# Kernel optimization log

Hardware: AMD Instinct MI355X
Metric: run time of the kernel (lower is better)

The kernel has to match this reference:

```python
import jax, jax.numpy as jnp
import numpy as np
from jax import lax

H = 12  # num_heads

def conv1d_same(x, w, b):
    # x: [B, Cin, L], w: [Cout, Cin, K] (torch Conv1d layout), 'same' padding
    y = lax.conv_general_dilated(x, w, window_strides=(1,), padding='SAME',
                                 dimension_numbers=('NCH', 'OIH', 'NCH'))
    return y + b[None, :, None]

def setup_inputs() -> dict:
    key = jax.random.key(0)
    ks = jax.random.split(key, 16)
    B, N, C = 8, 4096, 768
    d = C // H
    s = 0.02
    return {
        'x': jax.random.normal(ks[0], (B, N, C), dtype=jnp.float32),
        'qkv_w': jax.random.normal(ks[1], (3 * C, C), dtype=jnp.float32) * s,
        'proj_w': jax.random.normal(ks[2], (C, C), dtype=jnp.float32) * s,
        'proj_b': jnp.zeros((C,), dtype=jnp.float32),
        'conv_w': jax.random.normal(ks[3], (d, d, 5), dtype=jnp.float32) * s,  # k=5 from log2(768)
        'conv_b': jnp.zeros((d,), dtype=jnp.float32),
        'fc_w': jax.random.normal(ks[4], (d, d), dtype=jnp.float32) * s,
        'fc_b': jnp.zeros((d,), dtype=jnp.float32),
        'dw1_w': jax.random.normal(ks[5], (d, d, 3), dtype=jnp.float32) * s,
        'dw1_b': jnp.zeros((d,), dtype=jnp.float32),
        'dw2_w': jax.random.normal(ks[6], (d, d, 5), dtype=jnp.float32) * s,
        'dw2_b': jnp.zeros((d,), dtype=jnp.float32),
    }

def reference(x, qkv_w, proj_w, proj_b, conv_w, conv_b, fc_w, fc_b, dw1_w, dw1_b, dw2_w, dw2_b):
    B, N, C = x.shape
    d = C // H
    scale = d ** (-0.5)
    # qkv projection -> [3, B, H, N, d]
    qkv = (x @ qkv_w.T).reshape(B, N, 3, H, d).transpose(2, 0, 3, 1, 4)
    q, k, v = qkv[0], qkv[1], qkv[2]
    # SE-style gate: global avg over tokens, conv over channel axis, sigmoid
    res = jnp.mean(v, axis=2).reshape(B * H, d, 1)          # [BH, d, 1]
    res = conv1d_same(res, conv_w, conv_b)                   # [BH, d, 1]
    res = jax.nn.sigmoid(res).transpose(0, 2, 1).reshape(B, H, 1, d)
    # value branch: two 1D convs over token axis (channels = head_dim)
    vch = v.reshape(B * H, N, d).transpose(0, 2, 1)          # [BH, d, N]
    v2 = conv1d_same(vch, dw1_w, dw1_b) + conv1d_same(vch, dw2_w, dw2_b)
    v2 = v2.transpose(0, 2, 1).reshape(B, H, N, d)
    # channel attention: (scaled k)^T @ q -> [B, H, d, d]
    kq = jnp.einsum('bhnd,bhne->bhde', k * scale, q)
    a = jax.nn.relu(kq) @ fc_w.T + fc_b
    a = jax.nn.softmax(a + kq, axis=-1)
    # (a @ v2^T)^T -> [B, H, N, d]
    out = jnp.einsum('bhde,bhne->bhnd', a, v2)
    out = res * out
    out = out.transpose(0, 2, 1, 3).reshape(B, N, C)
    return out @ proj_w.T + proj_b
```

## Files before the change

kernel.cpp:

```cpp
#include <hip/hip_runtime.h>
#include <hip/hip_bf16.h>
#include <cstdint>
#include <cstddef>

typedef unsigned short u16;
typedef __attribute__((ext_vector_type(4))) unsigned short u16x4;
typedef __attribute__((ext_vector_type(8))) unsigned short u16x8;
typedef __attribute__((ext_vector_type(8))) short bf16x8;
typedef __attribute__((ext_vector_type(4))) float f32x4;

#define BB 8
#define NN 4096
#define CC 768
#define HH 12
#define DD 64
#define NHEADS 96
#define QKVSZ 25165824LL

__device__ inline float b2f(u16 u) { return __uint_as_float(((unsigned)u) << 16); }
__device__ inline u16 f2b(float f) {
    unsigned u = __float_as_uint(f);
    return (u16)((u + 0x7fffu + ((u >> 16) & 1u)) >> 16);
}
__device__ inline f32x4 zero4() { f32x4 z = {0.f, 0.f, 0.f, 0.f}; return z; }

__device__ __forceinline__ void gl_lds16(const u16* g, u16* l) {
    __builtin_amdgcn_global_load_lds(
        (const __attribute__((address_space(1))) void*)g,
        (__attribute__((address_space(3))) void*)l, 16, 0, 0);
}

__global__ void cast_all(const float* __restrict__ x, const float* __restrict__ w1,
                         const float* __restrict__ w2, u16* __restrict__ xb,
                         u16* __restrict__ wqkv, u16* __restrict__ wproj) {
    const long n0 = 25165824, n1 = 1769472, n2 = 589824;
    long i0 = (long)(blockIdx.x * blockDim.x + threadIdx.x) * 4;
    long stride = (long)gridDim.x * blockDim.x * 4;
    for (long j = i0; j < n0 + n1 + n2; j += stride) {
        const float* s; u16* d; long k;
        if (j < n0)            { s = x;  d = xb;    k = j; }
        else if (j < n0 + n1)  { s = w1; d = wqkv;  k = j - n0; }
        else                   { s = w2; d = wproj; k = j - n0 - n1; }
        float4 v = *(const float4*)(s + k);
        u16x4 o;
        o[0] = f2b(v.x); o[1] = f2b(v.y); o[2] = f2b(v.z); o[3] = f2b(v.w);
        *(u16x4*)(d + k) = o;
    }
}

template <int MODE>
__global__ __launch_bounds__(256) void gemm128d(const u16* __restrict__ A, const u16* __restrict__ Bm,
                                                const float* __restrict__ bias, void* __restrict__ out,
                                                int ncol) {
    constexpr int K = 768;
    __shared__ __align__(16) u16 lA[128 * 64];
    __shared__ __align__(16) u16 lB[128 * 64];
    const int tid = threadIdx.x;
    const int lane = tid & 63, wid = tid >> 6;
    const int wr = wid >> 1, wc = wid & 1;
    const int li = lane & 15, g = lane >> 4;

    const int nwg = gridDim.x, chunk = nwg >> 3;
    const int swz = ((int)blockIdx.x & 7) * chunk + ((int)blockIdx.x >> 3);
    const int col0 = (swz % ncol) * 128;
    const int row0 = (swz / ncol) * 128;

    const int lrow = lane >> 3;
    const int lcolsw = (((lane & 7) ^ lrow) * 8);

    f32x4 acc[4][4];
#pragma unroll
    for (int i = 0; i < 4; ++i)
#pragma unroll
        for (int j = 0; j < 4; ++j) acc[i][j] = zero4();

    for (int kt = 0; kt < K; kt += 64) {
#pragma unroll
        for (int s = 0; s < 4; ++s) {
            int r0 = wid * 32 + s * 8;
            gl_lds16(A  + (size_t)(row0 + r0 + lrow) * K + kt + lcolsw, lA + r0 * 64);
            gl_lds16(Bm + (size_t)(col0 + r0 + lrow) * K + kt + lcolsw, lB + r0 * 64);
        }
        __syncthreads();
#pragma unroll
        for (int kk = 0; kk < 64; kk += 32) {
            int kc = kk * 2 + (g << 4);
            bf16x8 af[4], bf_[4];
#pragma unroll
            for (int i = 0; i < 4; ++i) {
                int ra = wr * 64 + i * 16 + li;
                af[i] = *(const bf16x8*)((char*)lA + ((ra * 128 + kc) ^ ((ra & 7) << 4)));
                int rb = wc * 64 + i * 16 + li;
                bf_[i] = *(const bf16x8*)((char*)lB + ((rb * 128 + kc) ^ ((rb & 7) << 4)));
            }
#pragma unroll
            for (int i = 0; i < 4; ++i)
#pragma unroll
                for (int j = 0; j < 4; ++j)
                    acc[i][j] = __builtin_amdgcn_mfma_f32_16x16x32_bf16(af[i], bf_[j], acc[i][j], 0, 0, 0);
        }
        __syncthreads();
    }

#pragma unroll
    for (int i = 0; i < 4; ++i) {
#pragma unroll
        for (int j = 0; j < 4; ++j) {
            int c = col0 + wc * 64 + j * 16 + li;
            if constexpr (MODE == 0) {
                int part = c / 768, rem = c % 768;
                int h = rem >> 6, dd = rem & 63;
#pragma unroll
                for (int e = 0; e < 4; ++e) {
                    int r = row0 + wr * 64 + i * 16 + g * 4 + e;
                    int b = r >> 12, n = r & 4095;
                    ((u16*)out)[(((size_t)part * NHEADS + b * HH + h) * NN + n) * DD + dd] =
                        f2b(acc[i][j][e]);
                }
            } else {
                float bb = bias[c];
#pragma unroll
                for (int e = 0; e < 4; ++e) {
                    int r = row0 + wr * 64 + i * 16 + g * 4 + e;
                    ((float*)out)[(size_t)r * 768 + c] = acc[i][j][e] + bb;
                }
            }
        }
    }
}

__global__ __launch_bounds__(256) void kq_mean(const u16* __restrict__ qkv, float* __restrict__ kqp,
                                               float* __restrict__ meanp) {
    const int head = blockIdx.x, part = blockIdx.y;
    const int tid = threadIdx.x, lane = tid & 63, wid = tid >> 6;
    __shared__ __align__(16) u16 tiles[4][2][32 * 64];
    __shared__ float sred[16 * 64];

    if (part == 4) {
        const u16* vh = qkv + 2 * QKVSZ + (size_t)head * NN * DD;
        int rg = tid >> 4, cg = tid & 15;
        float s0 = 0.f, s1 = 0.f, s2 = 0.f, s3 = 0.f;
        for (int it = 0; it < 256; ++it) {
            int n = rg + it * 16;
            u16x4 v = *(const u16x4*)(vh + (size_t)n * DD + cg * 4);
            s0 += b2f(v[0]); s1 += b2f(v[1]); s2 += b2f(v[2]); s3 += b2f(v[3]);
        }
        sred[rg * 64 + cg * 4 + 0] = s0;
        sred[rg * 64 + cg * 4 + 1] = s1;
        sred[rg * 64 + cg * 4 + 2] = s2;
        sred[rg * 64 + cg * 4 + 3] = s3;
        __syncthreads();
        if (tid < 64) {
            float s = 0.f;
#pragma unroll
            for (int rg2 = 0; rg2 < 16; ++rg2) s += sred[rg2 * 64 + tid];
            meanp[head * 64 + tid] = s;
        }
        return;
    }

    u16* kt = tiles[wid][0];
    u16* qt = tiles[wid][1];
    const u16* qh = qkv + (size_t)head * NN * DD;
    const u16* kh = qkv + QKVSZ + (size_t)head * NN * DD;
    const int nbase = part * 1024 + wid * 256;

    f32x4 acc[4][4];
#pragma unroll
    for (int i = 0; i < 4; ++i)
#pragma unroll
        for (int j = 0; j < 4; ++j) acc[i][j] = zero4();

    const int srow = lane >> 3, schunk = (lane & 7) * 8;
    const int g8 = (lane >> 4) * 8, li = lane & 15;

    for (int it = 0; it < 8; ++it) {
        int n0 = nbase + it * 32;
#pragma unroll
        for (int p = 0; p < 4; ++p) {
            int r = srow + p * 8;
            *(u16x8*)(kt + r * 64 + schunk) = *(const u16x8*)(kh + (size_t)(n0 + r) * DD + schunk);
            *(u16x8*)(qt + r * 64 + schunk) = *(const u16x8*)(qh + (size_t)(n0 + r) * DD + schunk);
        }
        bf16x8 af[4], bf_[4];
#pragma unroll
        for (int i = 0; i < 4; ++i)
#pragma unroll
            for (int j = 0; j < 8; ++j) af[i][j] = (short)kt[(g8 + j) * 64 + i * 16 + li];
#pragma unroll
        for (int i = 0; i < 4; ++i)
#pragma unroll
            for (int j = 0; j < 8; ++j) bf_[i][j] = (short)qt[(g8 + j) * 64 + i * 16 + li];
#pragma unroll
        for (int i = 0; i < 4; ++i)
#pragma unroll
            for (int j = 0; j < 4; ++j)
                acc[i][j] = __builtin_amdgcn_mfma_f32_16x16x32_bf16(af[i], bf_[j], acc[i][j], 0, 0, 0);
    }

    const int slot = part * 4 + wid;
    const int g = lane >> 4;
    float* dst = kqp + ((size_t)head * 16 + slot) * 4096;
#pragma unroll
    for (int i = 0; i < 4; ++i)
#pragma unroll
        for (int j = 0; j < 4; ++j)
#pragma unroll
            for (int e = 0; e < 4; ++e)
                dst[(i * 16 + g * 4 + e) * 64 + j * 16 + li] = acc[i][j][e];
}

__global__ __launch_bounds__(256) void head_soft(
    const float* __restrict__ kqp, const float* __restrict__ meanp,
    const float* __restrict__ conv_w, const float* __restrict__ conv_b,
    const float* __restrict__ fc_w, const float* __restrict__ fc_b,
    const float* __restrict__ dw1_b, const float* __restrict__ dw2_b,
    float* __restrict__ sa_g, float* __restrict__ gate_g, float* __restrict__ effb) {
    const int head = blockIdx.x;
    const int tid = threadIdx.x;
    __shared__ float skq[64 * 64];
    __shared__ float sa[64 * 64];
    __shared__ float sgate[64];

    for (int idx = tid; idx < 4096; idx += 256) {
        float s = 0.f;
#pragma unroll
        for (int p = 0; p < 16; ++p) s += kqp[((size_t)head * 16 + p) * 4096 + idx];
        skq[idx] = s * 0.125f;
    }
    __syncthreads();
    if (tid < 64) {
        float gsum = conv_b[tid];
        for (int i = 0; i < 64; ++i)
            gsum += conv_w[(tid * 64 + i) * 5 + 2] * (meanp[head * 64 + i] * (1.f / 4096.f));
        float gt = 1.f / (1.f + __expf(-gsum));
        sgate[tid] = gt;
        gate_g[head * 64 + tid] = gt;
    }

    {
        int rr = tid >> 2, cg = (tid & 3) * 16;
        for (int c = cg; c < cg + 16; ++c) {
            float s = fc_b[c];
            for (int e = 0; e < 64; ++e) s += fmaxf(skq[rr * 64 + e], 0.f) * fc_w[c * 64 + e];
            sa[rr * 64 + c] = s + skq[rr * 64 + c];
        }
    }
    __syncthreads();
    if (tid < 64) {
        float m = -1e30f;
        for (int e = 0; e < 64; ++e) m = fmaxf(m, sa[tid * 64 + e]);
        float s = 0.f;
        for (int e = 0; e < 64; ++e) {
            float p = __expf(sa[tid * 64 + e] - m);
            sa[tid * 64 + e] = p;
            s += p;
        }
        float inv = 1.f / s;
        for (int e = 0; e < 64; ++e) sa[tid * 64 + e] *= inv;
    }
    __syncthreads();
    for (int idx = tid; idx < 4096; idx += 256) sa_g[(size_t)head * 4096 + idx] = sa[idx];
    if (tid < 64) {
        float s = 0.f;
        for (int e = 0; e < 64; ++e) s += sa[tid * 64 + e] * (dw1_b[e] + dw2_b[e]);
        effb[head * 64 + tid] = sgate[tid] * s;
    }
}

__global__ __launch_bounds__(256) void fold_eff(
    const float* __restrict__ sa_g, const float* __restrict__ gate_g,
    const float* __restrict__ dw1_w, const float* __restrict__ dw2_w,
    u16* __restrict__ eff) {
    const int head = blockIdx.x, ig = blockIdx.y;
    const int tid = threadIdx.x;
    __shared__ float ssa[4096];
    __shared__ float sw2[64 * 16 * 5];
    __shared__ float sw1[64 * 16 * 3];

    for (int idx = tid; idx < 4096; idx += 256) ssa[idx] = sa_g[(size_t)head * 4096 + idx];
    for (int idx = tid; idx < 64 * 16 * 5; idx += 256) {
        int e = idx / 80, rem = idx % 80, il = rem / 5, t = rem % 5;
        sw2[idx] = dw2_w[((size_t)(e * 64 + ig * 16 + il)) * 5 + t];
    }
    for (int idx = tid; idx < 64 * 16 * 3; idx += 256) {
        int e = idx / 48, rem = idx % 48, il = rem / 3, t = rem % 3;
        sw1[idx] = dw1_w[((size_t)(e * 64 + ig * 16 + il)) * 3 + t];
    }
    __syncthreads();

    const int il = tid & 15, og = tid >> 4;
    const int i = ig * 16 + il;
    float t[4][5];
#pragma unroll
    for (int o = 0; o < 4; ++o)
#pragma unroll
        for (int tp = 0; tp < 5; ++tp) t[o][tp] = 0.f;

    for (int e = 0; e < 64; ++e) {
        float a0 = ssa[(og * 4 + 0) * 64 + e];
        float a1 = ssa[(og * 4 + 1) * 64 + e];
        float a2 = ssa[(og * 4 + 2) * 64 + e];
        float a3 = ssa[(og * 4 + 3) * 64 + e];
        const float* w2 = sw2 + (e * 16 + il) * 5;
        const float* w1 = sw1 + (e * 16 + il) * 3;
        float c0 = w2[0], c1 = w2[1] + w1[0], c2 = w2[2] + w1[1], c3 = w2[3] + w1[2], c4 = w2[4];
        t[0][0] += a0 * c0; t[0][1] += a0 * c1; t[0][2] += a0 * c2; t[0][3] += a0 * c3; t[0][4] += a0 * c4;
        t[1][0] += a1 * c0; t[1][1] += a1 * c1; t[1][2] += a1 * c2; t[1][3] += a1 * c3; t[1][4] += a1 * c4;
        t[2][0] += a2 * c0; t[2][1] += a2 * c1; t[2][2] += a2 * c2; t[2][3] += a2 * c3; t[2][4] += a2 * c4;
        t[3][0] += a3 * c0; t[3][1] += a3 * c1; t[3][2] += a3 * c2; t[3][3] += a3 * c3; t[3][4] += a3 * c4;
    }
#pragma unroll
    for (int o = 0; o < 4; ++o) {
        int oo = og * 4 + o;
        float gt = gate_g[head * 64 + oo];
        u16* eo = eff + ((size_t)head * 64 + oo) * 320 + i;
#pragma unroll
        for (int tp = 0; tp < 5; ++tp) eo[tp * 64] = f2b(gt * t[o][tp]);
    }
}

__global__ __launch_bounds__(256) void conv_attn(const u16* __restrict__ qkv, const u16* __restrict__ eff,
                                                 const float* __restrict__ effb, u16* __restrict__ attn) {
    const int nt = blockIdx.x, head = blockIdx.y;
    const int tid = threadIdx.x, lane = tid & 63, wid = tid >> 6;
    __shared__ __align__(16) u16 vt[132 * 64];
    const int n0 = nt * 128;
    const u16* vh = qkv + 2 * QKVSZ + (size_t)head * NN * DD;

    {
        int sr = tid >> 3, sc = (tid & 7) * 8;
#pragma unroll
        for (int p = 0; p < 5; ++p) {
            int r = sr + p * 32;
            if (r < 132) {
                int n = n0 - 2 + r;
                u16x8 v = {0, 0, 0, 0, 0, 0, 0, 0};
                if (n >= 0 && n < NN) v = *(const u16x8*)(vh + (size_t)n * DD + sc);
                *(u16x8*)((char*)vt + ((r * 128 + sc * 2) ^ ((r & 7) << 4))) = v;
            }
        }
    }
    __syncthreads();

    f32x4 acc[2][4];
#pragma unroll
    for (int s = 0; s < 2; ++s)
#pragma unroll
        for (int j = 0; j < 4; ++j) acc[s][j] = zero4();

    const u16* effh = eff + (size_t)head * 64 * 320;
    const int li = lane & 15, g = lane >> 4;
#pragma unroll
    for (int s = 0; s < 10; ++s) {
        int tap = s >> 1, half = s & 1;
        bf16x8 bfr[4];
#pragma unroll
        for (int nj = 0; nj < 4; ++nj)
            bfr[nj] = *(const bf16x8*)(effh + (size_t)(nj * 16 + li) * 320 + s * 32 + g * 8);
        int kc = half * 64 + g * 16;
#pragma unroll
        for (int sub = 0; sub < 2; ++sub) {
            int rr = wid * 32 + sub * 16 + li + tap;
            bf16x8 afr = *(const bf16x8*)((char*)vt + ((rr * 128 + kc) ^ ((rr & 7) << 4)));
#pragma unroll
            for (int nj = 0; nj < 4; ++nj)
                acc[sub][nj] = __builtin_amdgcn_mfma_f32_16x16x32_bf16(afr, bfr[nj], acc[sub][nj], 0, 0, 0);
        }
    }

    const int b = head / HH, h = head % HH;
#pragma unroll
    for (int sub = 0; sub < 2; ++sub)
#pragma unroll
        for (int nj = 0; nj < 4; ++nj) {
            int o = nj * 16 + li;
            float bb = effb[head * 64 + o];
#pragma unroll
            for (int e = 0; e < 4; ++e) {
                int m = wid * 32 + sub * 16 + g * 4 + e;
                size_t n = (size_t)n0 + m;
                attn[((size_t)b * NN + n) * CC + h * DD + o] = f2b(acc[sub][nj][e] + bb);
            }
        }
}

extern "C" void kernel_launch(void* const* d_in, const int* in_sizes, int n_in,
                              void* d_out, int out_size, void* d_ws, size_t ws_size,
                              hipStream_t stream) {
    const float* x      = (const float*)d_in[0];
    const float* qkv_w  = (const float*)d_in[1];
    const float* proj_w = (const float*)d_in[2];
    const float* proj_b = (const float*)d_in[3];
    const float* conv_w = (const float*)d_in[4];
    const float* conv_b = (const float*)d_in[5];
    const float* fc_w   = (const float*)d_in[6];
    const float* fc_b   = (const float*)d_in[7];
    const float* dw1_w  = (const float*)d_in[8];
    const float* dw1_b  = (const float*)d_in[9];
    const float* dw2_w  = (const float*)d_in[10];
    const float* dw2_b  = (const float*)d_in[11];

    char* ws = (char*)d_ws;
    u16* xb    = (u16*)(ws);
    u16* wqkv  = (u16*)(ws + 50331648);
    u16* wproj = (u16*)(ws + 53870592);
    u16* qkv   = (u16*)(ws + 55050240);
    u16* eff   = (u16*)(ws + 206045184);
    float* effb = (float*)(ws + 209977344);
    u16* attn  = (u16*)(ws + 210001920);

    float* kqp    = (float*)(ws);
    float* meanp  = (float*)(ws + 25165824);
    float* sa_g   = (float*)(ws + 25190400);
    float* gate_g = (float*)(ws + 26763264);

    float* out = (float*)d_out;

    cast_all<<<2048, 256, 0, stream>>>(x, qkv_w, proj_w, xb, wqkv, wproj);

    gemm128d<0><<<4608, 256, 0, stream>>>(xb, wqkv, nullptr, qkv, 18);

    kq_mean<<<dim3(96, 5), 256, 0, stream>>>(qkv, kqp, meanp);
    head_soft<<<96, 256, 0, stream>>>(kqp, meanp, conv_w, conv_b, fc_w, fc_b,
                                      dw1_b, dw2_b, sa_g, gate_g, effb);
    fold_eff<<<dim3(96, 4), 256, 0, stream>>>(sa_g, gate_g, dw1_w, dw2_w, eff);

    conv_attn<<<dim3(32, 96), 256, 0, stream>>>(qkv, eff, effb, attn);

    gemm128d<1><<<1536, 256, 0, stream>>>(attn, wproj, proj_b, out, 6);
}
```

Measured before the change: 392.4 us.

## Use 256x256 double-buffered 8-wave GEMM for the QKV projection

Result: slower. 427.9 us (+9.1%).

```diff
diff --git a/kernel.cpp b/kernel.cpp
--- a/kernel.cpp
+++ b/kernel.cpp
@@ -49,6 +49,146 @@
 }
 
 template <int MODE>
+__global__ __launch_bounds__(512, 2) void gemm256p(const u16* __restrict__ A, const u16* __restrict__ Bm,
+                                                   const float* __restrict__ bias, void* __restrict__ out,
+                                                   int ncol) {
+    constexpr int K = 768;
+    constexpr int NT = K / 64;
+    constexpr int NI = NT / 2;
+    __shared__ __align__(16) u16 lA[2][256 * 64];
+    __shared__ __align__(16) u16 lB[2][256 * 64];
+    const int tid = threadIdx.x;
+    const int lane = tid & 63, wid = tid >> 6;
+    const int wr = wid >> 2, wc = wid & 3;
+    const int li = lane & 15, g = lane >> 4;
+
+    const int nwg = gridDim.x, chunk = nwg >> 3;
+    const int swz = ((int)blockIdx.x & 7) * chunk + ((int)blockIdx.x >> 3);
+    const int col0 = (swz % ncol) * 256;
+    const int row0 = (swz / ncol) * 256;
+
+    const int lrow = lane >> 3;
+    const int lcolsw = ((lane & 7) ^ lrow) * 8;
+
+    f32x4 acc[8][4];
+#pragma unroll
+    for (int i = 0; i < 8; ++i)
+#pragma unroll
+        for (int j = 0; j < 4; ++j) acc[i][j] = zero4();
+
+    auto stA = [&](int h, int tau) {
+        const int rb = h * 128 + wid * 16;
+        u16* dst = &lA[tau & 1][rb * 64];
+        const u16* src = A + (size_t)(row0 + rb + lrow) * K + tau * 64 + lcolsw;
+        gl_lds16(src, dst);
+        gl_lds16(src + (size_t)8 * K, dst + 8 * 64);
+    };
+    auto stB = [&](int h, int tau) {
+        const int rb = h * 128 + wid * 16;
+        u16* dst = &lB[tau & 1][rb * 64];
+        const u16* src = Bm + (size_t)(col0 + rb + lrow) * K + tau * 64 + lcolsw;
+        gl_lds16(src, dst);
+        gl_lds16(src + (size_t)8 * K, dst + 8 * 64);
+    };
+    auto quad = [&](int tau, int mh, int nh) {
+        const char* baseA = (const char*)&lA[tau & 1][0];
+        const char* baseB = (const char*)&lB[tau & 1][0];
+        bf16x8 bfr[2][2];
+#pragma unroll
+        for (int jj = 0; jj < 2; ++jj) {
+            int rb = nh * 128 + wc * 32 + jj * 16 + li;
+#pragma unroll
+            for (int k2 = 0; k2 < 2; ++k2)
+                bfr[jj][k2] = *(const bf16x8*)(baseB + ((rb * 128 + k2 * 64 + g * 16) ^ ((rb & 7) << 4)));
+        }
+        __builtin_amdgcn_s_setprio(1);
+#pragma unroll
+        for (int ii = 0; ii < 4; ++ii) {
+            int ra = mh * 128 + wr * 64 + ii * 16 + li;
+            bf16x8 af0 = *(const bf16x8*)(baseA + ((ra * 128 + g * 16) ^ ((ra & 7) << 4)));
+            bf16x8 af1 = *(const bf16x8*)(baseA + ((ra * 128 + 64 + g * 16) ^ ((ra & 7) << 4)));
+#pragma unroll
+            for (int jj = 0; jj < 2; ++jj) {
+                acc[mh * 4 + ii][nh * 2 + jj] =
+                    __builtin_amdgcn_mfma_f32_16x16x32_bf16(af0, bfr[jj][0], acc[mh * 4 + ii][nh * 2 + jj], 0, 0, 0);
+                acc[mh * 4 + ii][nh * 2 + jj] =
+                    __builtin_amdgcn_mfma_f32_16x16x32_bf16(af1, bfr[jj][1], acc[mh * 4 + ii][nh * 2 + jj], 0, 0, 0);
+            }
+        }
+        __builtin_amdgcn_s_setprio(0);
+    };
+#define FENCE_BAR() do { asm volatile("" ::: "memory"); __builtin_amdgcn_s_barrier(); } while (0)
+
+    stA(0, 0); stB(1, 0); stA(1, 0); stB(0, 0);
+    stA(0, 1); stB(1, 1);
+
+    for (int I = 0; I < NI; ++I) {
+        const int te = 2 * I, to = te + 1;
+        const bool lastI = (I == NI - 1);
+        asm volatile("s_waitcnt vmcnt(4)" ::: "memory");
+        __builtin_amdgcn_s_barrier();
+        stA(1, to);
+        quad(te, 0, 0);
+        FENCE_BAR();
+        stB(0, to);
+        quad(te, 0, 1);
+        FENCE_BAR();
+        if (!lastI) stA(0, te + 2);
+        quad(te, 1, 1);
+        FENCE_BAR();
+        if (!lastI) stB(1, te + 2);
+        quad(te, 1, 0);
+        FENCE_BAR();
+        if (lastI) { asm volatile("s_waitcnt vmcnt(0)" ::: "memory"); }
+        else       { asm volatile("s_waitcnt vmcnt(4)" ::: "memory"); }
+        __builtin_amdgcn_s_barrier();
+        if (!lastI) stA(1, te + 2);
+        quad(to, 0, 0);
+        FENCE_BAR();
+        if (!lastI) stB(0, te + 2);
+        quad(to, 0, 1);
+        FENCE_BAR();
+        if (to + 2 < NT) stA(0, to + 2);
+        quad(to, 1, 1);
+        FENCE_BAR();
+        if (to + 2 < NT) stB(1, to + 2);
+        quad(to, 1, 0);
+        FENCE_BAR();
+    }
+#undef FENCE_BAR
+
+#pragma unroll
+    for (int mh = 0; mh < 2; ++mh)
+#pragma unroll
+    for (int ii = 0; ii < 4; ++ii) {
+#pragma unroll
+        for (int nh = 0; nh < 2; ++nh)
+#pragma unroll
+        for (int jj = 0; jj < 2; ++jj) {
+            int c = col0 + nh * 128 + wc * 32 + jj * 16 + li;
+            f32x4 a = acc[mh * 4 + ii][nh * 2 + jj];
+            if constexpr (MODE == 0) {
+                int part = c / 768, rem = c % 768;
+                int h = rem >> 6, dd = rem & 63;
+#pragma unroll
+                for (int e = 0; e < 4; ++e) {
+                    int r = row0 + mh * 128 + wr * 64 + ii * 16 + g * 4 + e;
+                    int b = r >> 12, n = r & 4095;
+                    ((u16*)out)[(((size_t)part * NHEADS + b * HH + h) * NN + n) * DD + dd] = f2b(a[e]);
+                }
+            } else {
+                float bb = bias[c];
+#pragma unroll
+                for (int e = 0; e < 4; ++e) {
+                    int r = row0 + mh * 128 + wr * 64 + ii * 16 + g * 4 + e;
+                    ((float*)out)[(size_t)r * 768 + c] = a[e] + bb;
+                }
+            }
+        }
+    }
+}
+
+template <int MODE>
 __global__ __launch_bounds__(256) void gemm128d(const u16* __restrict__ A, const u16* __restrict__ Bm,
                                                 const float* __restrict__ bias, void* __restrict__ out,
                                                 int ncol) {
@@ -419,7 +559,7 @@
 
     cast_all<<<2048, 256, 0, stream>>>(x, qkv_w, proj_w, xb, wqkv, wproj);
 
-    gemm128d<0><<<4608, 256, 0, stream>>>(xb, wqkv, nullptr, qkv, 18);
+    gemm256p<0><<<1152, 512, 0, stream>>>(xb, wqkv, nullptr, qkv, 9);
 
     kq_mean<<<dim3(96, 5), 256, 0, stream>>>(qkv, kqp, meanp);
     head_soft<<<96, 256, 0, stream>>>(kqp, meanp, conv_w, conv_b, fc_w, fc_b,
```
